# Performance work log

Measured on AMD Instinct MI355X. Metric: run time of the kernel, lower is better.

## Reference

```python
import jax, jax.numpy as jnp
import numpy as np

INPUT_WINDOW = 2048
HEAD_DIM = 128  # embedding_size // number_of_heads = 2048 // 16
TAU = 1.0
SCALE = 1.0 / ((INPUT_WINDOW * HEAD_DIM) ** 0.5 * TAU)


def setup_inputs() -> dict:
    key = jax.random.key(0)
    # (batch, number_of_series, length_input_window, hidden_dimensionality)
    x = jax.random.normal(key, (8, 16, 2048, 128), dtype=jnp.float32)
    return {"x": x}


def reference(x) -> jnp.ndarray:
    # Q = K = V = x; scores: [B, S, W, W]
    qk = jnp.einsum("bswd,bsud->bswu", x, x) * SCALE
    attn = jax.nn.softmax(qk, axis=-1)
    # dropout(p=0.1) is identity in eval mode
    out = jnp.einsum("bswu,bsud->bswd", attn, x)
    return out
```

## Files before the change

### kernel.cpp

```cpp
#include <hip/hip_runtime.h>
#include <hip/hip_bf16.h>


#define NSEQ   2048
#define DIM    128
#define KVBLK  32
#define TILES  (NSEQ / KVBLK)
#define IMG    (KVBLK * DIM)
#define EC (1.44269504088896f / 512.0f)

typedef short s8v __attribute__((ext_vector_type(8)));
typedef float f4   __attribute__((ext_vector_type(4)));
typedef float f16v __attribute__((ext_vector_type(16)));
typedef unsigned int u2 __attribute__((ext_vector_type(2)));
typedef unsigned int u4 __attribute__((ext_vector_type(4)));

typedef __attribute__((address_space(1))) const void glob_t;
typedef __attribute__((address_space(3))) void lds_t;

__device__ __forceinline__ unsigned pk2(float a, float b) {
    union { __hip_bfloat162 h; unsigned u; } c;
    c.h = __float22bfloat162_rn(make_float2(a, b));
    return c.u;
}
__device__ __forceinline__ int swz32k(int r) { return ((r & 7) ^ ((r >> 3) & 3)) << 3; }
__device__ __forceinline__ int swz(int r) { return ((r & 7) ^ ((r >> 3) & 7)) << 3; }

__global__ __launch_bounds__(256)
void prepass(const float* __restrict__ x, short* __restrict__ wsK,
             short* __restrict__ wsV) {
    const int b = blockIdx.x;
    const float* src = x + (size_t)b * (64 * DIM);
    short* dK = wsK + (size_t)b * 2 * IMG;
    short* dV = wsV + (size_t)b * 2 * IMG;
    const int rw = threadIdx.x >> 4;
    const int cg = threadIdx.x & 15;
    const int tile = rw >> 3;
    const int ul   = 4 * (rw & 7);

    f4 ld[8];
    const float* s = src + (size_t)(4 * rw) * DIM + 8 * cg;
#pragma unroll
    for (int i = 0; i < 4; ++i) {
        ld[2*i]   = *(const f4*)(s + i * DIM);
        ld[2*i+1] = *(const f4*)(s + i * DIM + 4);
    }
#pragma unroll
    for (int i = 0; i < 4; ++i) {
        const int rl = ul + i;
        u4 kv = { pk2(ld[2*i][0],   ld[2*i][1]),   pk2(ld[2*i][2],   ld[2*i][3]),
                  pk2(ld[2*i+1][0], ld[2*i+1][1]), pk2(ld[2*i+1][2], ld[2*i+1][3]) };
        *(u4*)&dK[tile * IMG + ((rl * DIM + 8 * cg) ^ swz32k(rl))] = kv;
    }
#pragma unroll
    for (int j = 0; j < 8; ++j) {
        const int d  = 8 * cg + j;
        const int hi = j >> 2, jj = j & 3;
        u2 vv = { pk2(ld[0 + hi][jj], ld[2 + hi][jj]),
                  pk2(ld[4 + hi][jj], ld[6 + hi][jj]) };
        *(u2*)&dV[tile * IMG + ((d * KVBLK + ul) ^ swz32k(d))] = vv;
    }
}

__global__ __launch_bounds__(256, 3)
void attn_k32(const float* __restrict__ x, const short* __restrict__ wsK,
              const short* __restrict__ wsV, float* __restrict__ out) {
    const int bid  = blockIdx.x;
    const int wg   = (bid & 7) * 256 + (bid >> 3);
    const int head = wg >> 4;
    const int qb   = wg & 15;

    const float* __restrict__ xh = x   + (size_t)head * (NSEQ * DIM);
    float* __restrict__       oh = out + (size_t)head * (NSEQ * DIM);
    const short* gK = wsK + (size_t)head * TILES * IMG;
    const short* gV = wsV + (size_t)head * TILES * IMG;

    const int tid  = threadIdx.x;
    const int lane = tid & 63;
    const int wave = tid >> 6;
    const int l31  = lane & 31;
    const int h    = lane >> 5;

    __shared__ __align__(16) short sK [2][IMG];
    __shared__ __align__(16) short sVt[2][IMG];

    const int qw0 = qb * 128 + wave * 32;
    s8v Qf[8];
    {
        const float* qp = xh + (size_t)(qw0 + l31) * DIM + 8 * h;
#pragma unroll
        for (int ks = 0; ks < 8; ++ks) {
            f4 a = *(const f4*)(qp + ks * 16);
            f4 b = *(const f4*)(qp + ks * 16 + 4);
            u4 q = { pk2(a[0] * EC, a[1] * EC), pk2(a[2] * EC, a[3] * EC),
                     pk2(b[0] * EC, b[1] * EC), pk2(b[2] * EC, b[3] * EC) };
            Qf[ks] = *(s8v*)&q;
        }
    }

    f16v accO[4];
#pragma unroll
    for (int dt = 0; dt < 4; ++dt) accO[dt] = (f16v)(0.f);
    float lsum = 0.f;

    auto stage = [&](int b, int t) {
        const short* srcK = gK + (size_t)t * IMG;
        const short* srcV = gV + (size_t)t * IMG;
        const int off = wave * 1024 + lane * 8;
#pragma unroll
        for (int i = 0; i < 2; ++i) {
            __builtin_amdgcn_global_load_lds((glob_t*)(srcK + off + i * 512),
                (lds_t*)&sK[b][off + i * 512], 16, 0, 0);
            __builtin_amdgcn_global_load_lds((glob_t*)(srcV + off + i * 512),
                (lds_t*)&sVt[b][off + i * 512], 16, 0, 0);
        }
    };

    stage(0, 0);
    __syncthreads();
    int buf = 0;

    for (int t = 0; t < TILES; ++t) {
        if (t + 1 < TILES) stage(buf ^ 1, t + 1);

        f16v accS = (f16v)(0.f);
        {
            const int base = l31 * DIM + 8 * h;
            const int sz   = swz32k(l31);
            __builtin_amdgcn_s_setprio(1);
#pragma unroll
            for (int ks = 0; ks < 8; ++ks) {
                s8v Kf = *(const s8v*)&sK[buf][(base + ks * 16) ^ sz];
                accS = __builtin_amdgcn_mfma_f32_32x32x16_bf16(Kf, Qf[ks], accS, 0, 0, 0);
            }
            __builtin_amdgcn_s_setprio(0);
        }

        float part = 0.f;
#pragma unroll
        for (int r = 0; r < 16; ++r) {
            float v = __builtin_amdgcn_exp2f(accS[r]);
            accS[r] = v;
            part += v;
        }
        lsum += part;

        s8v Pf[2];
#pragma unroll
        for (int ksl = 0; ksl < 2; ++ksl) {
            unsigned pa0 = pk2(accS[8*ksl + 0], accS[8*ksl + 1]);
            unsigned pa1 = pk2(accS[8*ksl + 2], accS[8*ksl + 3]);
            unsigned pb0 = pk2(accS[8*ksl + 4], accS[8*ksl + 5]);
            unsigned pb1 = pk2(accS[8*ksl + 6], accS[8*ksl + 7]);
            auto t0 = __builtin_amdgcn_permlane32_swap(pa0, pb0, false, false);
            auto t1 = __builtin_amdgcn_permlane32_swap(pa1, pb1, false, false);
            u4 w = { (unsigned)t0[0], (unsigned)t1[0], (unsigned)t0[1], (unsigned)t1[1] };
            Pf[ksl] = *(s8v*)&w;
        }

        __builtin_amdgcn_s_setprio(1);
#pragma unroll
        for (int dt = 0; dt < 4; ++dt) {
            const int d    = dt * 32 + l31;
            const int base = d * KVBLK + 8 * h;
            const int sz   = swz32k(d);
#pragma unroll
            for (int ksl = 0; ksl < 2; ++ksl) {
                s8v Vf = *(const s8v*)&sVt[buf][(base + ksl * 16) ^ sz];
                accO[dt] = __builtin_amdgcn_mfma_f32_32x32x16_bf16(
                    Pf[ksl], Vf, accO[dt], 0, 0, 0);
            }
        }
        __builtin_amdgcn_s_setprio(0);

        __syncthreads();
        buf ^= 1;
    }

    const float tot = lsum + __shfl_xor(lsum, 32);
    const float inv = 1.f / tot;
#pragma unroll
    for (int r = 0; r < 16; ++r) {
        const int q      = (r & 3) + 8 * (r >> 2) + 4 * h;
        const float invq = __shfl(inv, q, 32);
        float* op = oh + (size_t)(qw0 + q) * DIM + l31;
#pragma unroll
        for (int dt = 0; dt < 4; ++dt)
            op[dt * 32] = accO[dt][r] * invq;
    }
}

__global__ __launch_bounds__(256, 2)
void attn_fwd_fb(const float* __restrict__ x, float* __restrict__ out) {
    const int bid  = blockIdx.x;
    const int wg   = (bid & 7) * 256 + (bid >> 3);
    const int head = wg >> 4;
    const int qb   = wg & 15;
    const float* __restrict__ xh = x   + (size_t)head * (NSEQ * DIM);
    float* __restrict__       oh = out + (size_t)head * (NSEQ * DIM);
    const int tid  = threadIdx.x;
    const int lane = tid & 63;
    const int wave = tid >> 6;
    const int l31  = lane & 31;
    const int h    = lane >> 5;
    __shared__ __align__(16) short sK [64 * DIM];
    __shared__ __align__(16) short sVt[DIM * 64];
    const int qw0 = qb * 128 + wave * 32;
    s8v Qf[8];
    {
        const float* qp = xh + (size_t)(qw0 + l31) * DIM + 8 * h;
#pragma unroll
        for (int ks = 0; ks < 8; ++ks) {
            f4 a = *(const f4*)(qp + ks * 16);
            f4 b = *(const f4*)(qp + ks * 16 + 4);
            u4 q = { pk2(a[0] * EC, a[1] * EC), pk2(a[2] * EC, a[3] * EC),
                     pk2(b[0] * EC, b[1] * EC), pk2(b[2] * EC, b[3] * EC) };
            Qf[ks] = *(s8v*)&q;
        }
    }
    f16v accO[4];
#pragma unroll
    for (int dt = 0; dt < 4; ++dt) accO[dt] = (f16v)(0.f);
    float lsum = 0.f;
    const int rw = tid >> 4;
    const int cg = tid & 15;
    f4 ld[8];
    {
        const float* s = xh + (size_t)(4 * rw) * DIM + 8 * cg;
#pragma unroll
        for (int i = 0; i < 4; ++i) {
            ld[2*i]   = *(const f4*)(s + i * DIM);
            ld[2*i+1] = *(const f4*)(s + i * DIM + 4);
        }
    }
    for (int kv0 = 0; kv0 < NSEQ; kv0 += 64) {
#pragma unroll
        for (int i = 0; i < 4; ++i) {
            const int r = 4 * rw + i;
            u4 kv = { pk2(ld[2*i][0],   ld[2*i][1]),   pk2(ld[2*i][2],   ld[2*i][3]),
                      pk2(ld[2*i+1][0], ld[2*i+1][1]), pk2(ld[2*i+1][2], ld[2*i+1][3]) };
            *(u4*)&sK[(r * DIM + 8 * cg) ^ swz(r)] = kv;
        }
#pragma unroll
        for (int j = 0; j < 8; ++j) {
            const int d  = 8 * cg + j;
            const int hi = j >> 2, jj = j & 3;
            u2 vv = { pk2(ld[0 + hi][jj], ld[2 + hi][jj]),
                      pk2(ld[4 + hi][jj], ld[6 + hi][jj]) };
            *(u2*)&sVt[(d * 64 + 4 * rw) ^ swz(d)] = vv;
        }
        __syncthreads();
        f16v accS[2];
        accS[0] = (f16v)(0.f); accS[1] = (f16v)(0.f);
        __builtin_amdgcn_s_setprio(1);
#pragma unroll
        for (int ut = 0; ut < 2; ++ut) {
            const int r    = ut * 32 + l31;
            const int base = r * DIM + 8 * h;
            const int sz   = swz(r);
#pragma unroll
            for (int ks = 0; ks < 8; ++ks) {
                s8v Kf = *(const s8v*)&sK[(base + ks * 16) ^ sz];
                accS[ut] = __builtin_amdgcn_mfma_f32_32x32x16_bf16(
                    Kf, Qf[ks], accS[ut], 0, 0, 0);
            }
        }
        __builtin_amdgcn_s_setprio(0);
        if (kv0 + 64 < NSEQ) {
            const float* s = xh + (size_t)(kv0 + 64 + 4 * rw) * DIM + 8 * cg;
#pragma unroll
            for (int i = 0; i < 4; ++i) {
                ld[2*i]   = *(const f4*)(s + i * DIM);
                ld[2*i+1] = *(const f4*)(s + i * DIM + 4);
            }
        }
        float part = 0.f;
#pragma unroll
        for (int ut = 0; ut < 2; ++ut)
#pragma unroll
            for (int r = 0; r < 16; ++r) {
                float v = __builtin_amdgcn_exp2f(accS[ut][r]);
                accS[ut][r] = v;
                part += v;
            }
        lsum += part;
        s8v Pf[4];
#pragma unroll
        for (int ks = 0; ks < 4; ++ks) {
#define PP(f) accS[(f) >> 4][(f) & 15]
            unsigned pa0 = pk2(PP(8*ks + 0), PP(8*ks + 1));
            unsigned pa1 = pk2(PP(8*ks + 2), PP(8*ks + 3));
            unsigned pb0 = pk2(PP(8*ks + 4), PP(8*ks + 5));
            unsigned pb1 = pk2(PP(8*ks + 6), PP(8*ks + 7));
#undef PP
            auto t0 = __builtin_amdgcn_permlane32_swap(pa0, pb0, false, false);
            auto t1 = __builtin_amdgcn_permlane32_swap(pa1, pb1, false, false);
            u4 w = { (unsigned)t0[0], (unsigned)t1[0], (unsigned)t0[1], (unsigned)t1[1] };
            Pf[ks] = *(s8v*)&w;
        }
        __builtin_amdgcn_s_setprio(1);
#pragma unroll
        for (int dt = 0; dt < 4; ++dt) {
            const int d    = dt * 32 + l31;
            const int base = d * 64 + 8 * h;
            const int sz   = swz(d);
#pragma unroll
            for (int ks = 0; ks < 4; ++ks) {
                s8v Vf = *(const s8v*)&sVt[(base + ks * 16) ^ sz];
                accO[dt] = __builtin_amdgcn_mfma_f32_32x32x16_bf16(
                    Pf[ks], Vf, accO[dt], 0, 0, 0);
            }
        }
        __builtin_amdgcn_s_setprio(0);
        __syncthreads();
    }
    const float tot = lsum + __shfl_xor(lsum, 32);
    const float inv = 1.f / tot;
#pragma unroll
    for (int r = 0; r < 16; ++r) {
        const int q      = (r & 3) + 8 * (r >> 2) + 4 * h;
        const float invq = __shfl(inv, q, 32);
        float* op = oh + (size_t)(qw0 + q) * DIM + l31;
#pragma unroll
        for (int dt = 0; dt < 4; ++dt)
            op[dt * 32] = accO[dt][r] * invq;
    }
}

extern "C" void kernel_launch(void* const* d_in, const int* in_sizes, int n_in,
                              void* d_out, int out_size, void* d_ws, size_t ws_size,
                              hipStream_t stream) {
    const float* x = (const float*)d_in[0];
    float* out     = (float*)d_out;
    const size_t perImg = (size_t)128 * TILES * IMG;
    const size_t need   = 2 * perImg * sizeof(short);
    if (ws_size >= need) {
        short* wsK = (short*)d_ws;
        short* wsV = wsK + perImg;
        hipLaunchKernelGGL(prepass, dim3(4096), dim3(256), 0, stream, x, wsK, wsV);
        hipLaunchKernelGGL(attn_k32, dim3(2048), dim3(256), 0, stream, x, wsK, wsV, out);
    } else {
        hipLaunchKernelGGL(attn_fwd_fb, dim3(2048), dim3(256), 0, stream, x, out);
    }
}
```

Baseline: 353.2 us.

## Process two 32-row query tiles per wave to reuse K/V LDS fragments

Each wave now handles 64 query rows (two 32-row MFMA tiles) instead of 32, so every K and V fragment read from LDS feeds two MFMAs. The block covers 256 queries and the grid halves to 1024 blocks, which halves the K/V staging traffic per query. In exchange it roughly doubles the accumulator registers, drops the occupancy hint from 3 to 2 blocks per CU, and leaves fewer blocks to balance across CUs.

New measurement: 436.5 us. 23.6% more time.

```diff
diff --git a/kernel.cpp b/kernel.cpp
--- a/kernel.cpp
+++ b/kernel.cpp
@@ -62,16 +62,15 @@
     }
 }
 
-__global__ __launch_bounds__(256, 3)
-void attn_k32(const float* __restrict__ x, const short* __restrict__ wsK,
+__global__ __launch_bounds__(256, 2)
+void attn_q64(const float* __restrict__ x, const short* __restrict__ wsK,
               const short* __restrict__ wsV, float* __restrict__ out) {
     const int bid  = blockIdx.x;
-    const int wg   = (bid & 7) * 256 + (bid >> 3);
-    const int head = wg >> 4;
-    const int qb   = wg & 15;
-
-    const float* __restrict__ xh = x   + (size_t)head * (NSEQ * DIM);
-    float* __restrict__       oh = out + (size_t)head * (NSEQ * DIM);
+    const int wg   = (bid & 7) * 128 + (bid >> 3);
+    const int head = wg >> 3;
+    const int qb   = wg & 7;
+
+    float* __restrict__ oh = out + (size_t)head * (NSEQ * DIM);
     const short* gK = wsK + (size_t)head * TILES * IMG;
     const short* gV = wsV + (size_t)head * TILES * IMG;
 
@@ -84,35 +83,41 @@
     __shared__ __align__(16) short sK [2][IMG];
     __shared__ __align__(16) short sVt[2][IMG];
 
-    const int qw0 = qb * 128 + wave * 32;
-    s8v Qf[8];
+    const int qw0 = qb * 256 + wave * 64;
+    s8v Qf0[8], Qf1[8];
     {
-        const float* qp = xh + (size_t)(qw0 + l31) * DIM + 8 * h;
-#pragma unroll
-        for (int ks = 0; ks < 8; ++ks) {
-            f4 a = *(const f4*)(qp + ks * 16);
-            f4 b = *(const f4*)(qp + ks * 16 + 4);
-            u4 q = { pk2(a[0] * EC, a[1] * EC), pk2(a[2] * EC, a[3] * EC),
-                     pk2(b[0] * EC, b[1] * EC), pk2(b[2] * EC, b[3] * EC) };
-            Qf[ks] = *(s8v*)&q;
-        }
-    }
-
-    f16v accO[4];
-#pragma unroll
-    for (int dt = 0; dt < 4; ++dt) accO[dt] = (f16v)(0.f);
-    float lsum = 0.f;
-
+        const float* xh = x + (size_t)head * (NSEQ * DIM);
+#pragma unroll
+        for (int qt = 0; qt < 2; ++qt) {
+            const float* qp = xh + (size_t)(qw0 + qt * 32 + l31) * DIM + 8 * h;
+#pragma unroll
+            for (int ks = 0; ks < 8; ++ks) {
+                f4 a = *(const f4*)(qp + ks * 16);
+                f4 b = *(const f4*)(qp + ks * 16 + 4);
+                u4 q = { pk2(a[0] * EC, a[1] * EC), pk2(a[2] * EC, a[3] * EC),
+                         pk2(b[0] * EC, b[1] * EC), pk2(b[2] * EC, b[3] * EC) };
+                if (qt == 0) Qf0[ks] = *(s8v*)&q; else Qf1[ks] = *(s8v*)&q;
+            }
+        }
+    }
+
+    f16v accO[2][4];
+#pragma unroll
+    for (int qt = 0; qt < 2; ++qt)
+#pragma unroll
+        for (int dt = 0; dt < 4; ++dt) accO[qt][dt] = (f16v)(0.f);
+    float lsum0 = 0.f, lsum1 = 0.f;
+
+    const int soff = wave * 1024 + lane * 8;
     auto stage = [&](int b, int t) {
-        const short* srcK = gK + (size_t)t * IMG;
-        const short* srcV = gV + (size_t)t * IMG;
-        const int off = wave * 1024 + lane * 8;
+        const short* srcK = gK + (size_t)t * IMG + soff;
+        const short* srcV = gV + (size_t)t * IMG + soff;
 #pragma unroll
         for (int i = 0; i < 2; ++i) {
-            __builtin_amdgcn_global_load_lds((glob_t*)(srcK + off + i * 512),
-                (lds_t*)&sK[b][off + i * 512], 16, 0, 0);
-            __builtin_amdgcn_global_load_lds((glob_t*)(srcV + off + i * 512),
-                (lds_t*)&sVt[b][off + i * 512], 16, 0, 0);
+            __builtin_amdgcn_global_load_lds((glob_t*)(srcK + i * 512),
+                (lds_t*)&sK[b][soff + i * 512], 16, 0, 0);
+            __builtin_amdgcn_global_load_lds((glob_t*)(srcV + i * 512),
+                (lds_t*)&sVt[b][soff + i * 512], 16, 0, 0);
         }
     };
 
@@ -120,42 +125,64 @@
     __syncthreads();
     int buf = 0;
 
+    const int kbase = l31 * DIM + 8 * h;
+    const int ksz   = swz32k(l31);
+
     for (int t = 0; t < TILES; ++t) {
         if (t + 1 < TILES) stage(buf ^ 1, t + 1);
 
-        f16v accS = (f16v)(0.f);
+        f16v accS0 = (f16v)(0.f), accS1 = (f16v)(0.f);
+        __builtin_amdgcn_s_setprio(1);
+#pragma unroll
+        for (int ks = 0; ks < 8; ++ks) {
+            s8v Kf = *(const s8v*)&sK[buf][(kbase + ks * 16) ^ ksz];
+            accS0 = __builtin_amdgcn_mfma_f32_32x32x16_bf16(Kf, Qf0[ks], accS0, 0, 0, 0);
+            accS1 = __builtin_amdgcn_mfma_f32_32x32x16_bf16(Kf, Qf1[ks], accS1, 0, 0, 0);
+        }
+        __builtin_amdgcn_s_setprio(0);
+
+        s8v Pf0[2], Pf1[2];
         {
-            const int base = l31 * DIM + 8 * h;
-            const int sz   = swz32k(l31);
-            __builtin_amdgcn_s_setprio(1);
-#pragma unroll
-            for (int ks = 0; ks < 8; ++ks) {
-                s8v Kf = *(const s8v*)&sK[buf][(base + ks * 16) ^ sz];
-                accS = __builtin_amdgcn_mfma_f32_32x32x16_bf16(Kf, Qf[ks], accS, 0, 0, 0);
-            }
-            __builtin_amdgcn_s_setprio(0);
-        }
-
-        float part = 0.f;
-#pragma unroll
-        for (int r = 0; r < 16; ++r) {
-            float v = __builtin_amdgcn_exp2f(accS[r]);
-            accS[r] = v;
-            part += v;
-        }
-        lsum += part;
-
-        s8v Pf[2];
-#pragma unroll
-        for (int ksl = 0; ksl < 2; ++ksl) {
-            unsigned pa0 = pk2(accS[8*ksl + 0], accS[8*ksl + 1]);
-            unsigned pa1 = pk2(accS[8*ksl + 2], accS[8*ksl + 3]);
-            unsigned pb0 = pk2(accS[8*ksl + 4], accS[8*ksl + 5]);
-            unsigned pb1 = pk2(accS[8*ksl + 6], accS[8*ksl + 7]);
-            auto t0 = __builtin_amdgcn_permlane32_swap(pa0, pb0, false, false);
-            auto t1 = __builtin_amdgcn_permlane32_swap(pa1, pb1, false, false);
-            u4 w = { (unsigned)t0[0], (unsigned)t1[0], (unsigned)t0[1], (unsigned)t1[1] };
-            Pf[ksl] = *(s8v*)&w;
+            float part = 0.f;
+#pragma unroll
+            for (int r = 0; r < 16; ++r) {
+                float v = __builtin_amdgcn_exp2f(accS0[r]);
+                accS0[r] = v;
+                part += v;
+            }
+            lsum0 += part;
+#pragma unroll
+            for (int ksl = 0; ksl < 2; ++ksl) {
+                unsigned pa0 = pk2(accS0[8*ksl + 0], accS0[8*ksl + 1]);
+                unsigned pa1 = pk2(accS0[8*ksl + 2], accS0[8*ksl + 3]);
+                unsigned pb0 = pk2(accS0[8*ksl + 4], accS0[8*ksl + 5]);
+                unsigned pb1 = pk2(accS0[8*ksl + 6], accS0[8*ksl + 7]);
+                auto t0 = __builtin_amdgcn_permlane32_swap(pa0, pb0, false, false);
+                auto t1 = __builtin_amdgcn_permlane32_swap(pa1, pb1, false, false);
+                u4 w = { (unsigned)t0[0], (unsigned)t1[0], (unsigned)t0[1], (unsigned)t1[1] };
+                Pf0[ksl] = *(s8v*)&w;
+            }
+        }
+        {
+            float part = 0.f;
+#pragma unroll
+            for (int r = 0; r < 16; ++r) {
+                float v = __builtin_amdgcn_exp2f(accS1[r]);
+                accS1[r] = v;
+                part += v;
+            }
+            lsum1 += part;
+#pragma unroll
+            for (int ksl = 0; ksl < 2; ++ksl) {
+                unsigned pa0 = pk2(accS1[8*ksl + 0], accS1[8*ksl + 1]);
+                unsigned pa1 = pk2(accS1[8*ksl + 2], accS1[8*ksl + 3]);
+                unsigned pb0 = pk2(accS1[8*ksl + 4], accS1[8*ksl + 5]);
+                unsigned pb1 = pk2(accS1[8*ksl + 6], accS1[8*ksl + 7]);
+                auto t0 = __builtin_amdgcn_permlane32_swap(pa0, pb0, false, false);
+                auto t1 = __builtin_amdgcn_permlane32_swap(pa1, pb1, false, false);
+                u4 w = { (unsigned)t0[0], (unsigned)t1[0], (unsigned)t0[1], (unsigned)t1[1] };
+                Pf1[ksl] = *(s8v*)&w;
+            }
         }
 
         __builtin_amdgcn_s_setprio(1);
@@ -167,8 +194,10 @@
 #pragma unroll
             for (int ksl = 0; ksl < 2; ++ksl) {
                 s8v Vf = *(const s8v*)&sVt[buf][(base + ksl * 16) ^ sz];
-                accO[dt] = __builtin_amdgcn_mfma_f32_32x32x16_bf16(
-                    Pf[ksl], Vf, accO[dt], 0, 0, 0);
+                accO[0][dt] = __builtin_amdgcn_mfma_f32_32x32x16_bf16(
+                    Pf0[ksl], Vf, accO[0][dt], 0, 0, 0);
+                accO[1][dt] = __builtin_amdgcn_mfma_f32_32x32x16_bf16(
+                    Pf1[ksl], Vf, accO[1][dt], 0, 0, 0);
             }
         }
         __builtin_amdgcn_s_setprio(0);
@@ -177,16 +206,20 @@
         buf ^= 1;
     }
 
-    const float tot = lsum + __shfl_xor(lsum, 32);
-    const float inv = 1.f / tot;
-#pragma unroll
-    for (int r = 0; r < 16; ++r) {
-        const int q      = (r & 3) + 8 * (r >> 2) + 4 * h;
-        const float invq = __shfl(inv, q, 32);
-        float* op = oh + (size_t)(qw0 + q) * DIM + l31;
-#pragma unroll
-        for (int dt = 0; dt < 4; ++dt)
-            op[dt * 32] = accO[dt][r] * invq;
+#pragma unroll
+    for (int qt = 0; qt < 2; ++qt) {
+        const float ls  = qt ? lsum1 : lsum0;
+        const float tot = ls + __shfl_xor(ls, 32);
+        const float inv = 1.f / tot;
+#pragma unroll
+        for (int r = 0; r < 16; ++r) {
+            const int q      = (r & 3) + 8 * (r >> 2) + 4 * h;
+            const float invq = __shfl(inv, q, 32);
+            float* op = oh + (size_t)(qw0 + qt * 32 + q) * DIM + l31;
+#pragma unroll
+            for (int dt = 0; dt < 4; ++dt)
+                op[dt * 32] = accO[qt][dt][r] * invq;
+        }
     }
 }
 
@@ -338,7 +371,7 @@
         short* wsK = (short*)d_ws;
         short* wsV = wsK + perImg;
         hipLaunchKernelGGL(prepass, dim3(4096), dim3(256), 0, stream, x, wsK, wsV);
-        hipLaunchKernelGGL(attn_k32, dim3(2048), dim3(256), 0, stream, x, wsK, wsV, out);
+        hipLaunchKernelGGL(attn_q64, dim3(1024), dim3(256), 0, stream, x, wsK, wsV, out);
     } else {
         hipLaunchKernelGGL(attn_fwd_fb, dim3(2048), dim3(256), 0, stream, x, out);
     }
```
